# Performance work log

Measured on AMD Instinct MI355X. Metric: run time of the kernel, lower is better.

## Reference

```python
import jax, jax.numpy as jnp
import numpy as np

NUM_CLASSES = 10
CLAUSES_PER_CLASS = 100  # first half vote positive, second half negative
M = NUM_CLASSES * CLAUSES_PER_CLASS  # 1000 clauses
D = 1152   # 2*C*kh*kw literals (pos+neg) per patch
L = 676    # patches (26x26)
B = 64
MASK_DENSITY = 0.01  # ~11 selected literals per clause


def setup_inputs() -> dict:
    key = jax.random.key(0)
    k1, k2, k3 = jax.random.split(key, 3)
    # binary literals in {0,1}
    literals = jax.random.randint(k1, (B, D, L), 0, 2, dtype=jnp.int32)
    # fixed discrete clause definitions: sparse boolean selection over D literals
    clause_mask = jax.random.uniform(k2, (M, D)) < MASK_DENSITY
    # per-clause vote weight alpha (learnable parameter in the torch module)
    alpha = 1.0 + 0.1 * jax.random.normal(k3, (M,), dtype=jnp.float32)
    return {"literals": literals, "clause_mask": clause_mask, "alpha": alpha}


def reference(literals, clause_mask, alpha):
    # literals: [B, D, L] in {0,1}; clause_mask: [M, D] bool; alpha: [M]
    lits = literals.astype(jnp.float32)
    mask = clause_mask.astype(jnp.float32)
    # AND over selected literals: clause m fires at patch l iff every selected
    # literal is 1  <=>  sum of selected literal values == number selected.
    sel_count = jnp.einsum('md,bdl->bml', mask, lits)      # [B, M, L]
    n_sel = mask.sum(axis=1)                               # [M]
    fired = sel_count >= n_sel[None, :, None]              # [B, M, L] bool (empty clause fires)
    # OR across patches
    or_patches = jnp.any(fired, axis=2).astype(alpha.dtype)  # [B, M]
    # weighted vote: per class, first half of its clauses vote +, second half -
    weighted = (or_patches * alpha[None, :]).reshape(-1, NUM_CLASSES, CLAUSES_PER_CLASS)
    half = CLAUSES_PER_CLASS // 2
    sign = jnp.concatenate([jnp.ones((half,), jnp.float32),
                            -jnp.ones((half,), jnp.float32)])
    scores = (weighted * sign).sum(axis=-1)                # [B, num_classes]
    return scores
```

## Files before the change

kernel.cpp:

```cpp
#include <hip/hip_runtime.h>
#include <hip/hip_bf16.h>
#include <stdint.h>

#define NUM_CLASSES 10
#define CPC 100
#define M_CLAUSES 1000
#define D_LITS 1152
#define L_PATCHES 676
#define BATCH 64
#define KMAX 64
#define NPACK_BLK 18432
#define NDET_BLK 64

typedef unsigned long long u64;

__global__ __launch_bounds__(256) void pack_kernel(
    const int* __restrict__ lits,
    const unsigned int* __restrict__ mask_u32,
    ulonglong2* __restrict__ packed,
    int* __restrict__ flags,
    float* __restrict__ out)
{
  int bid = blockIdx.x;
  if (bid < NPACK_BLK) {
    int wib  = threadIdx.x >> 6;
    int lane = threadIdx.x & 63;
    int row  = bid * 4 + wib;
    int b = row / D_LITS;
    int d = row - b * D_LITS;
    const int4* src = (const int4*)(lits + (size_t)row * L_PATCHES);
    u64 w0,w1,w2,w3,w4,w5,w6,w7,w8,w9,w10,w11;
    {
      int4 v = src[lane];
      w0 = __ballot(v.x != 0); w1 = __ballot(v.y != 0);
      w2 = __ballot(v.z != 0); w3 = __ballot(v.w != 0);
    }
    {
      int4 v = src[64 + lane];
      w4 = __ballot(v.x != 0); w5 = __ballot(v.y != 0);
      w6 = __ballot(v.z != 0); w7 = __ballot(v.w != 0);
    }
    {
      int4 v = make_int4(0,0,0,0);
      if (lane < 41) v = src[128 + lane];
      w8 = __ballot(v.x != 0); w9 = __ballot(v.y != 0);
      w10 = __ballot(v.z != 0); w11 = __ballot(v.w != 0);
    }
    ulonglong2* dst = packed + (size_t)d * 6 * 64 + b;
    if      (lane == 0) dst[0*64] = make_ulonglong2(w0,  w1);
    else if (lane == 1) dst[1*64] = make_ulonglong2(w2,  w3);
    else if (lane == 2) dst[2*64] = make_ulonglong2(w4,  w5);
    else if (lane == 3) dst[3*64] = make_ulonglong2(w6,  w7);
    else if (lane == 4) dst[4*64] = make_ulonglong2(w8,  w9);
    else if (lane == 5) dst[5*64] = make_ulonglong2(w10, w11);
  } else if (bid < NPACK_BLK + NDET_BLK) {
    int db = bid - NPACK_BLK;
    __shared__ int sfound;
    if (threadIdx.x == 0) sfound = 0;
    __syncthreads();
    int n = (M_CLAUSES * D_LITS) / 4;
    int found = 0;
    for (int i = db * 256 + threadIdx.x; i < n; i += NDET_BLK * 256)
      if (mask_u32[i] & 0xFFFFFF00u) found = 1;
    if (found) sfound = 1;
    __syncthreads();
    if (threadIdx.x == 0) flags[db] = sfound;
  } else {
    for (int i = threadIdx.x; i < BATCH * NUM_CLASSES; i += 256) out[i] = 0.f;
  }
}

__global__ __launch_bounds__(64) void score_kernel(
    const ulonglong2* __restrict__ packed,
    const void* __restrict__ maskp,
    const int* __restrict__ flags,
    const float* __restrict__ alpha,
    float* __restrict__ out)
{
  int m   = blockIdx.x;
  int tid = threadIdx.x;
  __shared__ int list[KMAX];
  __shared__ int cnt;
  __shared__ int isbool;
  if (tid == 0) {
    cnt = 0;
    int f = 0;
#pragma unroll
    for (int i = 0; i < NDET_BLK; ++i) f |= flags[i];
    isbool = f;
  }
  __syncthreads();
  bool ib = (isbool != 0);
  for (int d = tid; d < D_LITS; d += 64) {
    bool sel = ib ? (((const unsigned char*)maskp)[(size_t)m * D_LITS + d] != 0)
                  : (((const int*)maskp)[(size_t)m * D_LITS + d] != 0);
    if (sel) { int p = atomicAdd(&cnt, 1); if (p < KMAX) list[p] = d; }
  }
  __syncthreads();
  int c = cnt; if (c > KMAX) c = KMAX;
  const u64 TAIL = (1ull << 41) - 1;
  u64 a0=~0ull,a1=~0ull,a2=~0ull,a3=~0ull,a4=~0ull,a5=~0ull,a6=~0ull,a7=~0ull;
  u64 a8=TAIL, a9=TAIL, a10=TAIL, a11=TAIL;
  for (int k = 0; k < c; ++k) {
    int d = list[k];
    const ulonglong2* p = packed + (size_t)d * 6 * 64 + tid;
    ulonglong2 r0 = p[0*64], r1 = p[1*64], r2 = p[2*64];
    ulonglong2 r3 = p[3*64], r4 = p[4*64], r5 = p[5*64];
    a0 &= r0.x;  a1 &= r0.y;  a2 &= r1.x;  a3 &= r1.y;
    a4 &= r2.x;  a5 &= r2.y;  a6 &= r3.x;  a7 &= r3.y;
    a8 &= r4.x;  a9 &= r4.y;  a10 &= r5.x; a11 &= r5.y;
  }
  u64 any = (a0|a1|a2|a3)|(a4|a5|a6|a7)|(a8|a9|a10|a11);
  if (any) {
    float a = alpha[m];
    int cid = m / CPC;
    float v = ((m - cid * CPC) < (CPC / 2)) ? a : -a;
    atomicAdd(&out[tid * NUM_CLASSES + cid], v);
  }
}

extern "C" void kernel_launch(void* const* d_in, const int* in_sizes, int n_in,
                              void* d_out, int out_size, void* d_ws, size_t ws_size,
                              hipStream_t stream) {
  const int*   lits  = (const int*)d_in[0];
  const void*  mask  = d_in[1];
  const float* alpha = (const float*)d_in[2];
  float* out = (float*)d_out;

  char* ws = (char*)d_ws;
  int*        flags  = (int*)ws;
  ulonglong2* packed = (ulonglong2*)(ws + 4096);

  pack_kernel<<<NPACK_BLK + NDET_BLK + 1, 256, 0, stream>>>(
      lits, (const unsigned int*)mask, packed, flags, out);
  score_kernel<<<M_CLAUSES, 64, 0, stream>>>(packed, mask, flags, alpha, out);
}
```

Baseline: 296.9 us.

## Use nontemporal loads, larger pack blocks, vectorized mask scan, unrolled AND loop

The pack kernel now runs 512 threads with 8 waves per block and reads the int literal tensor with nontemporal loads, since the data streams through once. The packed store becomes a single predicated store instead of a chain of branches. The score kernel scans mask rows as 32-bit or int4 words instead of single elements, and unrolls the AND loop by two so more independent loads are in flight. The pack stage is bandwidth bound on about 200MB of reads, so the gains mostly depend on how the nontemporal hint behaves.

```diff
diff --git a/kernel.cpp b/kernel.cpp
--- a/kernel.cpp
+++ b/kernel.cpp
@@ -9,12 +9,22 @@
 #define L_PATCHES 676
 #define BATCH 64
 #define KMAX 64
-#define NPACK_BLK 18432
+#define WPB 8
+#define NPACK_BLK 9216
 #define NDET_BLK 64
 
 typedef unsigned long long u64;
 
-__global__ __launch_bounds__(256) void pack_kernel(
+static __device__ __forceinline__ int4 nt_load_int4(const int4* p) {
+  int4 r;
+  r.x = __builtin_nontemporal_load(&((const int*)p)[0]);
+  r.y = __builtin_nontemporal_load(&((const int*)p)[1]);
+  r.z = __builtin_nontemporal_load(&((const int*)p)[2]);
+  r.w = __builtin_nontemporal_load(&((const int*)p)[3]);
+  return r;
+}
+
+__global__ __launch_bounds__(512) void pack_kernel(
     const int* __restrict__ lits,
     const unsigned int* __restrict__ mask_u32,
     ulonglong2* __restrict__ packed,
@@ -25,34 +35,35 @@
   if (bid < NPACK_BLK) {
     int wib  = threadIdx.x >> 6;
     int lane = threadIdx.x & 63;
-    int row  = bid * 4 + wib;
+    int row  = bid * WPB + wib;
     int b = row / D_LITS;
     int d = row - b * D_LITS;
     const int4* src = (const int4*)(lits + (size_t)row * L_PATCHES);
     u64 w0,w1,w2,w3,w4,w5,w6,w7,w8,w9,w10,w11;
     {
-      int4 v = src[lane];
+      int4 v = nt_load_int4(src + lane);
       w0 = __ballot(v.x != 0); w1 = __ballot(v.y != 0);
       w2 = __ballot(v.z != 0); w3 = __ballot(v.w != 0);
     }
     {
-      int4 v = src[64 + lane];
+      int4 v = nt_load_int4(src + 64 + lane);
       w4 = __ballot(v.x != 0); w5 = __ballot(v.y != 0);
       w6 = __ballot(v.z != 0); w7 = __ballot(v.w != 0);
     }
     {
       int4 v = make_int4(0,0,0,0);
-      if (lane < 41) v = src[128 + lane];
+      if (lane < 41) v = nt_load_int4(src + 128 + lane);
       w8 = __ballot(v.x != 0); w9 = __ballot(v.y != 0);
       w10 = __ballot(v.z != 0); w11 = __ballot(v.w != 0);
     }
-    ulonglong2* dst = packed + (size_t)d * 6 * 64 + b;
-    if      (lane == 0) dst[0*64] = make_ulonglong2(w0,  w1);
-    else if (lane == 1) dst[1*64] = make_ulonglong2(w2,  w3);
-    else if (lane == 2) dst[2*64] = make_ulonglong2(w4,  w5);
-    else if (lane == 3) dst[3*64] = make_ulonglong2(w6,  w7);
-    else if (lane == 4) dst[4*64] = make_ulonglong2(w8,  w9);
-    else if (lane == 5) dst[5*64] = make_ulonglong2(w10, w11);
+    u64 lo = w0, hi = w1;
+    if (lane == 1) { lo = w2;  hi = w3;  }
+    if (lane == 2) { lo = w4;  hi = w5;  }
+    if (lane == 3) { lo = w6;  hi = w7;  }
+    if (lane == 4) { lo = w8;  hi = w9;  }
+    if (lane == 5) { lo = w10; hi = w11; }
+    if (lane < 6)
+      packed[(size_t)d * 384 + (size_t)lane * 64 + b] = make_ulonglong2(lo, hi);
   } else if (bid < NPACK_BLK + NDET_BLK) {
     int db = bid - NPACK_BLK;
     __shared__ int sfound;
@@ -60,13 +71,13 @@
     __syncthreads();
     int n = (M_CLAUSES * D_LITS) / 4;
     int found = 0;
-    for (int i = db * 256 + threadIdx.x; i < n; i += NDET_BLK * 256)
-      if (mask_u32[i] & 0xFFFFFF00u) found = 1;
+    for (int i = db * 512 + threadIdx.x; i < n; i += NDET_BLK * 512)
+      if (__builtin_nontemporal_load(mask_u32 + i) & 0xFFFFFF00u) found = 1;
     if (found) sfound = 1;
     __syncthreads();
     if (threadIdx.x == 0) flags[db] = sfound;
   } else {
-    for (int i = threadIdx.x; i < BATCH * NUM_CLASSES; i += 256) out[i] = 0.f;
+    if (threadIdx.x < BATCH * NUM_CLASSES) out[threadIdx.x] = 0.f;
   }
 }
 
@@ -90,22 +101,53 @@
     isbool = f;
   }
   __syncthreads();
-  bool ib = (isbool != 0);
-  for (int d = tid; d < D_LITS; d += 64) {
-    bool sel = ib ? (((const unsigned char*)maskp)[(size_t)m * D_LITS + d] != 0)
-                  : (((const int*)maskp)[(size_t)m * D_LITS + d] != 0);
-    if (sel) { int p = atomicAdd(&cnt, 1); if (p < KMAX) list[p] = d; }
+  if (isbool) {
+    const unsigned int* mrow = (const unsigned int*)maskp + (size_t)m * (D_LITS / 4);
+    for (int r = 0; r < 5; ++r) {
+      int i = r * 64 + tid;
+      if (i < D_LITS / 4) {
+        unsigned int v = mrow[i];
+        if (v) {
+#pragma unroll
+          for (int c4 = 0; c4 < 4; ++c4)
+            if ((v >> (8 * c4)) & 0xFF) { int p = atomicAdd(&cnt, 1); if (p < KMAX) list[p] = i * 4 + c4; }
+        }
+      }
+    }
+  } else {
+    const int4* mrow = (const int4*)((const int*)maskp + (size_t)m * D_LITS);
+    for (int r = 0; r < 5; ++r) {
+      int i = r * 64 + tid;
+      if (i < D_LITS / 4) {
+        int4 v = mrow[i];
+        if (v.x) { int p = atomicAdd(&cnt, 1); if (p < KMAX) list[p] = i * 4 + 0; }
+        if (v.y) { int p = atomicAdd(&cnt, 1); if (p < KMAX) list[p] = i * 4 + 1; }
+        if (v.z) { int p = atomicAdd(&cnt, 1); if (p < KMAX) list[p] = i * 4 + 2; }
+        if (v.w) { int p = atomicAdd(&cnt, 1); if (p < KMAX) list[p] = i * 4 + 3; }
+      }
+    }
   }
   __syncthreads();
   int c = cnt; if (c > KMAX) c = KMAX;
   const u64 TAIL = (1ull << 41) - 1;
   u64 a0=~0ull,a1=~0ull,a2=~0ull,a3=~0ull,a4=~0ull,a5=~0ull,a6=~0ull,a7=~0ull;
   u64 a8=TAIL, a9=TAIL, a10=TAIL, a11=TAIL;
-  for (int k = 0; k < c; ++k) {
-    int d = list[k];
-    const ulonglong2* p = packed + (size_t)d * 6 * 64 + tid;
-    ulonglong2 r0 = p[0*64], r1 = p[1*64], r2 = p[2*64];
-    ulonglong2 r3 = p[3*64], r4 = p[4*64], r5 = p[5*64];
+  int k = 0;
+  for (; k + 2 <= c; k += 2) {
+    const ulonglong2* p0 = packed + (size_t)list[k]     * 384 + tid;
+    const ulonglong2* p1 = packed + (size_t)list[k + 1] * 384 + tid;
+    ulonglong2 r0 = p0[0], r1 = p0[64], r2 = p0[128];
+    ulonglong2 r3 = p0[192], r4 = p0[256], r5 = p0[320];
+    ulonglong2 s0 = p1[0], s1 = p1[64], s2 = p1[128];
+    ulonglong2 s3 = p1[192], s4 = p1[256], s5 = p1[320];
+    a0 &= r0.x & s0.x;  a1 &= r0.y & s0.y;  a2 &= r1.x & s1.x;  a3 &= r1.y & s1.y;
+    a4 &= r2.x & s2.x;  a5 &= r2.y & s2.y;  a6 &= r3.x & s3.x;  a7 &= r3.y & s3.y;
+    a8 &= r4.x & s4.x;  a9 &= r4.y & s4.y;  a10 &= r5.x & s5.x; a11 &= r5.y & s5.y;
+  }
+  if (k < c) {
+    const ulonglong2* p0 = packed + (size_t)list[k] * 384 + tid;
+    ulonglong2 r0 = p0[0], r1 = p0[64], r2 = p0[128];
+    ulonglong2 r3 = p0[192], r4 = p0[256], r5 = p0[320];
     a0 &= r0.x;  a1 &= r0.y;  a2 &= r1.x;  a3 &= r1.y;
     a4 &= r2.x;  a5 &= r2.y;  a6 &= r3.x;  a7 &= r3.y;
     a8 &= r4.x;  a9 &= r4.y;  a10 &= r5.x; a11 &= r5.y;
@@ -131,7 +173,7 @@
   int*        flags  = (int*)ws;
   ulonglong2* packed = (ulonglong2*)(ws + 4096);
 
-  pack_kernel<<<NPACK_BLK + NDET_BLK + 1, 256, 0, stream>>>(
+  pack_kernel<<<NPACK_BLK + NDET_BLK + 1, 512, 0, stream>>>(
       lits, (const unsigned int*)mask, packed, flags, out);
   score_kernel<<<M_CLAUSES, 64, 0, stream>>>(packed, mask, flags, alpha, out);
 }
```

New measurement: 279.9 us. -5.7%, faster.
